# Performance work log

Hardware: AMD Instinct MI355X
Metric: run time of the kernel (lower is better)

Reference implementation:

```python
import jax, jax.numpy as jnp
import numpy as np

N = 10000        # num_nodes
E = 160000       # num_edges (before self loops)
D_IN = 256       # input_dim
H = 128          # hidden_dim (= per-head out_channels)
HEADS = 4
HD = HEADS * H   # 512
L = 16           # num_layers
OUT = 1024       # output_dim
G = 8            # num graphs in batch
EPS = 1e-5


def _layer_norm(x, w, b):
    m = jnp.mean(x, axis=-1, keepdims=True)
    v = jnp.mean(jnp.square(x - m), axis=-1, keepdims=True)
    return (x - m) / jnp.sqrt(v + EPS) * w + b


def setup_inputs() -> dict:
    key = jax.random.key(0)
    ks = jax.random.split(key, 20)
    s = 0.05
    x = jax.random.normal(ks[0], (N, D_IN), jnp.float32)
    edge_index = jax.random.randint(ks[1], (2, E), 0, N, dtype=jnp.int64)
    batch = jnp.sort(jax.random.randint(ks[2], (N,), 0, G, dtype=jnp.int64))
    return {
        "x": x,
        "edge_index": edge_index,
        "batch": batch,
        "W_in": jax.random.normal(ks[3], (D_IN, H), jnp.float32) * s,
        "b_in": jnp.zeros((H,), jnp.float32),
        "ln_in_w": jnp.ones((H,), jnp.float32),
        "ln_in_b": jnp.zeros((H,), jnp.float32),
        "Wsrc": jax.random.normal(ks[4], (L, H, HD), jnp.float32) * s,
        "Wdst": jax.random.normal(ks[5], (L, H, HD), jnp.float32) * s,
        "att_src": jax.random.normal(ks[6], (L, HEADS, H), jnp.float32) * s,
        "att_dst": jax.random.normal(ks[7], (L, HEADS, H), jnp.float32) * s,
        "Wout": jax.random.normal(ks[8], (L, HD, H), jnp.float32) * s,
        "bout": jnp.zeros((L, H), jnp.float32),
        "ln_w": jnp.ones((L, H), jnp.float32),
        "ln_b": jnp.zeros((L, H), jnp.float32),
        "Wp1": jax.random.normal(ks[9], (H, OUT), jnp.float32) * s,
        "bp1": jnp.zeros((OUT,), jnp.float32),
        "Wp2": jax.random.normal(ks[10], (OUT, OUT), jnp.float32) * s,
        "bp2": jnp.zeros((OUT,), jnp.float32),
    }


def reference(x, edge_index, batch, W_in, b_in, ln_in_w, ln_in_b,
              Wsrc, Wdst, att_src, att_dst, Wout, bout, ln_w, ln_b,
              Wp1, bp1, Wp2, bp2):
    # add self loops once (same edge set every layer)
    loop = jnp.arange(N, dtype=edge_index.dtype)
    e_src = jnp.concatenate([edge_index[0], loop])  # x_j (source)
    e_dst = jnp.concatenate([edge_index[1], loop])  # x_i (target / aggregate index)

    h = jax.nn.relu(_layer_norm(x @ W_in + b_in, ln_in_w, ln_in_b))  # [N, H]

    for l in range(L):
        hs = (h[e_src] @ Wsrc[l]).reshape(-1, HEADS, H)  # [E2, heads, H]
        hd = (h[e_dst] @ Wdst[l]).reshape(-1, HEADS, H)
        a = jnp.sum(hs * att_src[l], axis=-1) + jnp.sum(hd * att_dst[l], axis=-1)  # [E2, heads]
        a = jax.nn.leaky_relu(a, 0.2)
        # NOTE: faithful to source -- softmax over HEADS per edge, not over neighbors
        a = jax.nn.softmax(a, axis=-1)
        msg = (hs * a[..., None]).reshape(-1, HD)  # [E2, HD]
        agg = jax.ops.segment_sum(msg, e_dst, num_segments=N)  # [N, HD]
        out = agg @ Wout[l] + bout[l]
        h = jax.nn.relu(_layer_norm(out + h, ln_w[l], ln_b[l]))  # residual: H == H

    g = jax.ops.segment_max(h, batch, num_segments=G)  # global max pool [G, H]
    g = jax.nn.relu(g @ Wp1 + bp1)
    return g @ Wp2 + bp2  # [G, OUT]
```

## Files before the change

kernel.cpp:

```cpp
#include <hip/hip_runtime.h>
#include <hip/hip_bf16.h>

#define N_NODES 10000
#define E_EDGES 160000
#define E2 (E_EDGES + N_NODES)
#define D_IN 256
#define H 128
#define HEADS 4
#define HD 512
#define L_LAYERS 16
#define OUT_DIM 1024
#define G_GRAPHS 8
#define EPS 1e-5f
#define SPAD 10016

typedef unsigned short ushort_t;
typedef __attribute__((ext_vector_type(8))) short short8;
typedef __attribute__((ext_vector_type(4))) float f32x4;
typedef __attribute__((ext_vector_type(4))) unsigned u32x4;

__device__ __forceinline__ f32x4 mfma16(short8 a, short8 b, f32x4 c) {
    return __builtin_amdgcn_mfma_f32_16x16x32_bf16(a, b, c, 0, 0, 0);
}
__device__ __forceinline__ unsigned short f2b(float f) {
    unsigned u = __float_as_uint(f);
    u += 0x7fffu + ((u >> 16) & 1u);
    return (unsigned short)(u >> 16);
}
__device__ __forceinline__ float b2f(unsigned short b) {
    return __uint_as_float((unsigned)b << 16);
}
__device__ __forceinline__ unsigned pk2(float lo, float hi) {
    __hip_bfloat162 p = __float22bfloat162_rn(make_float2(lo, hi));
    return *(unsigned*)&p;
}

__global__ void k_zero(int* deg, int* cur, unsigned* g) {
    int i = blockIdx.x * blockDim.x + threadIdx.x;
    if (i < N_NODES) { deg[i] = 0; cur[i] = 0; }
    if (i < G_GRAPHS * H) g[i] = 0u;
}

__global__ void k_count(const int* ei, int* deg) {
    int e = blockIdx.x * blockDim.x + threadIdx.x;
    if (e >= E2) return;
    int d = (e < E_EDGES) ? ei[E_EDGES + e] : (e - E_EDGES);
    atomicAdd(&deg[d], 1);
}

__global__ void k_scan(const int* deg, int* rs) {
    __shared__ int s[1024];
    int t = threadIdx.x;
    int base = t * 10;
    int loc[10], run = 0;
    #pragma unroll
    for (int i = 0; i < 10; i++) {
        int idx = base + i;
        int v = (idx < N_NODES) ? deg[idx] : 0;
        loc[i] = run; run += v;
    }
    s[t] = run;
    __syncthreads();
    for (int off = 1; off < 1024; off <<= 1) {
        int xv = (t >= off) ? s[t - off] : 0;
        __syncthreads();
        s[t] += xv;
        __syncthreads();
    }
    int excl = s[t] - run;
    #pragma unroll
    for (int i = 0; i < 10; i++) {
        int idx = base + i;
        if (idx <= N_NODES) rs[idx] = excl + loc[i];
    }
}

__global__ void k_fill(const int* ei, const int* rs, int* cur, int* elist) {
    int e = blockIdx.x * blockDim.x + threadIdx.x;
    if (e >= E2) return;
    int s, d;
    if (e < E_EDGES) { s = ei[e]; d = ei[E_EDGES + e]; }
    else { s = d = e - E_EDGES; }
    int pos = atomicAdd(&cur[d], 1);
    elist[rs[d] + pos] = s;
}

__global__ void k_vw(const float* Wsrc, const float* Wdst,
                     const float* att_src, const float* att_dst,
                     float* vsrc, float* vdst) {
    int l = blockIdx.x;
    int t = threadIdx.x;
    int head = t >> 7, j = t & 127;
    const float* Ws = Wsrc + (size_t)l * H * HD;
    const float* Wd = Wdst + (size_t)l * H * HD;
    const float* As = att_src + (size_t)l * HEADS * H;
    const float* Ad = att_dst + (size_t)l * HEADS * H;
    float ss = 0.f, sd = 0.f;
    for (int k = 0; k < H; k++) {
        ss += Ws[(size_t)j * HD + head * H + k] * As[head * H + k];
        sd += Wd[(size_t)j * HD + head * H + k] * Ad[head * H + k];
    }
    vsrc[(size_t)l * HD + head * H + j] = ss;
    vdst[(size_t)l * HD + head * H + j] = sd;
}

__global__ __launch_bounds__(256) void k_mm(const float* __restrict__ Wsrc,
        const float* __restrict__ Wout, float* __restrict__ M) {
    __shared__ float As[32][33];
    __shared__ float Bs[32][128];
    int bid = blockIdx.x;
    int q = bid & 3, hh = (bid >> 2) & 3, l = bid >> 4;
    int t = threadIdx.x;
    int ty = t >> 4, tx = t & 15;
    const float* WsB = Wsrc + (size_t)l * H * HD + (size_t)hh * 128;
    const float* WoB = Wout + (size_t)l * HD * H + (size_t)hh * 128 * H;
    float acc[2][8];
    #pragma unroll
    for (int r = 0; r < 2; r++)
        #pragma unroll
        for (int c = 0; c < 8; c++) acc[r][c] = 0.f;
    for (int kt = 0; kt < 4; kt++) {
        #pragma unroll
        for (int i = 0; i < 4; i++) {
            int lin = i * 256 + t;
            int rr = lin >> 5, cc = lin & 31;
            As[rr][cc] = WsB[(size_t)(q * 32 + rr) * HD + kt * 32 + cc];
        }
        #pragma unroll
        for (int i = 0; i < 16; i++) {
            int lin = i * 256 + t;
            int rr = lin >> 7, cc = lin & 127;
            Bs[rr][cc] = WoB[(size_t)(kt * 32 + rr) * H + cc];
        }
        __syncthreads();
        #pragma unroll
        for (int kk = 0; kk < 32; kk++) {
            float a0 = As[ty * 2][kk], a1 = As[ty * 2 + 1][kk];
            float4 b0 = *(const float4*)&Bs[kk][tx * 8];
            float4 b1 = *(const float4*)&Bs[kk][tx * 8 + 4];
            acc[0][0] += a0 * b0.x; acc[0][1] += a0 * b0.y;
            acc[0][2] += a0 * b0.z; acc[0][3] += a0 * b0.w;
            acc[0][4] += a0 * b1.x; acc[0][5] += a0 * b1.y;
            acc[0][6] += a0 * b1.z; acc[0][7] += a0 * b1.w;
            acc[1][0] += a1 * b0.x; acc[1][1] += a1 * b0.y;
            acc[1][2] += a1 * b0.z; acc[1][3] += a1 * b0.w;
            acc[1][4] += a1 * b1.x; acc[1][5] += a1 * b1.y;
            acc[1][6] += a1 * b1.z; acc[1][7] += a1 * b1.w;
        }
        __syncthreads();
    }
    #pragma unroll
    for (int r = 0; r < 2; r++)
        #pragma unroll
        for (int c = 0; c < 8; c++)
            M[(size_t)l * HD * H + (size_t)(hh * 128 + q * 32 + ty * 2 + r) * H + tx * 8 + c]
                = acc[r][c];
}

__global__ void k_pack_out2(const float* M, ushort_t* Wh, ushort_t* Wl) {
    int idx = blockIdx.x * 256 + threadIdx.x;
    int l = idx >> 16, rem = idx & 65535;
    int k = rem >> 7, col = rem & 127;
    float v = M[(size_t)l * HD * H + (size_t)k * H + col];
    unsigned short hi = f2b(v);
    unsigned short lo = f2b(v - b2f(hi));
    int nt = col >> 4, ks = k >> 5, lhi = (k >> 3) & 3, llo = col & 15, j = k & 7;
    size_t addr = (size_t)l * 65536 + (((size_t)(nt * 16 + ks) * 64) + lhi * 16 + llo) * 8 + j;
    Wh[addr] = hi;
    Wl[addr] = lo;
}

__global__ void k_pack_win(const float* W, ushort_t* Wp) {
    int idx = blockIdx.x * 256 + threadIdx.x;
    int k = idx >> 7, col = idx & 127;
    float v = W[(size_t)k * H + col];
    int nt = col >> 4, ks = k >> 5, lhi = (k >> 3) & 3, llo = col & 15, j = k & 7;
    Wp[(((size_t)(nt * 8 + ks) * 64) + lhi * 16 + llo) * 8 + j] = f2b(v);
}

__global__ __launch_bounds__(256) void k_in_mfma(
        const float* __restrict__ x, const ushort_t* __restrict__ WpI,
        const float* __restrict__ b_in, const float* __restrict__ lnw,
        const float* __restrict__ lnb, const float* __restrict__ vs,
        const float* __restrict__ vd, float* __restrict__ as0, float* __restrict__ ad0,
        float* __restrict__ h, ushort_t* __restrict__ hb) {
    __shared__ float part1[4][16], part2[4][16];
    __shared__ float apart[4][8][16];
    int t = threadIdx.x, w = t >> 6, lane = t & 63;
    int row0 = blockIdx.x * 16;
    int ar = lane & 15, ac = (lane >> 4) * 8;
    short8 a[8];
    #pragma unroll
    for (int ks = 0; ks < 8; ks++) {
        const float* xp = x + (size_t)(row0 + ar) * D_IN + ks * 32 + ac;
        float4 xa = *(const float4*)xp;
        float4 xb = *(const float4*)(xp + 4);
        u32x4 u;
        u.x = pk2(xa.x, xa.y); u.y = pk2(xa.z, xa.w);
        u.z = pk2(xb.x, xb.y); u.w = pk2(xb.z, xb.w);
        a[ks] = *(short8*)&u;
    }
    const ushort_t* B0 = WpI + ((size_t)(w * 2 + 0) * 8) * 64 * 8;
    const ushort_t* B1 = WpI + ((size_t)(w * 2 + 1) * 8) * 64 * 8;
    f32x4 c0 = {0.f, 0.f, 0.f, 0.f}, c1 = {0.f, 0.f, 0.f, 0.f};
    #pragma unroll
    for (int ks = 0; ks < 8; ks++) {
        short8 b0 = *(const short8*)(B0 + ((size_t)ks * 64 + lane) * 8);
        short8 b1 = *(const short8*)(B1 + ((size_t)ks * 64 + lane) * 8);
        c0 = mfma16(a[ks], b0, c0);
        c1 = mfma16(a[ks], b1, c1);
    }
    int col0 = w * 32 + ar, col1 = w * 32 + 16 + ar;
    int rb = (lane >> 4) * 4;
    float v0[4], v1[4], y0[4], y1[4];
    #pragma unroll
    for (int r = 0; r < 4; r++) {
        v0[r] = c0[r] + b_in[col0];
        v1[r] = c1[r] + b_in[col1];
        float p1 = v0[r] + v1[r];
        float p2 = v0[r] * v0[r] + v1[r] * v1[r];
        #pragma unroll
        for (int off = 1; off < 16; off <<= 1) {
            p1 += __shfl_xor(p1, off);
            p2 += __shfl_xor(p2, off);
        }
        if (ar == 0) { part1[w][rb + r] = p1; part2[w][rb + r] = p2; }
    }
    __syncthreads();
    #pragma unroll
    for (int r = 0; r < 4; r++) {
        int lr = rb + r;
        int row = row0 + lr;
        float s1 = part1[0][lr] + part1[1][lr] + part1[2][lr] + part1[3][lr];
        float s2 = part2[0][lr] + part2[1][lr] + part2[2][lr] + part2[3][lr];
        float m = s1 * (1.f / 128.f);
        float var = s2 * (1.f / 128.f) - m * m;
        float is = rsqrtf(var + EPS);
        y0[r] = fmaxf((v0[r] - m) * is * lnw[col0] + lnb[col0], 0.f);
        y1[r] = fmaxf((v1[r] - m) * is * lnw[col1] + lnb[col1], 0.f);
        h[(size_t)row * H + col0] = y0[r];
        h[(size_t)row * H + col1] = y1[r];
        hb[(size_t)row * H + col0] = f2b(y0[r]);
        hb[(size_t)row * H + col1] = f2b(y1[r]);
    }
    #pragma unroll
    for (int comp = 0; comp < 8; comp++) {
        float vc0 = (comp < 4) ? vs[comp * H + col0] : vd[(comp - 4) * H + col0];
        float vc1 = (comp < 4) ? vs[comp * H + col1] : vd[(comp - 4) * H + col1];
        float p[4];
        #pragma unroll
        for (int r = 0; r < 4; r++) p[r] = y0[r] * vc0 + y1[r] * vc1;
        #pragma unroll
        for (int off = 1; off < 16; off <<= 1)
            #pragma unroll
            for (int r = 0; r < 4; r++) p[r] += __shfl_xor(p[r], off);
        if (ar == 0)
            #pragma unroll
            for (int r = 0; r < 4; r++) apart[w][comp][rb + r] = p[r];
    }
    __syncthreads();
    if (t < 128) {
        int lr = t >> 3, comp = t & 7;
        float s = apart[0][comp][lr] + apart[1][comp][lr]
                + apart[2][comp][lr] + apart[3][comp][lr];
        int node = row0 + lr;
        if (comp < 4) as0[node * 4 + comp] = s;
        else          ad0[node * 4 + comp - 4] = s;
    }
}

#define ACC1(uv, wt) do { \
    acc[0] += (wt) * __uint_as_float((uv).x << 16); \
    acc[1] += (wt) * __uint_as_float((uv).x & 0xffff0000u); \
    acc[2] += (wt) * __uint_as_float((uv).y << 16); \
    acc[3] += (wt) * __uint_as_float((uv).y & 0xffff0000u); \
    acc[4] += (wt) * __uint_as_float((uv).z << 16); \
    acc[5] += (wt) * __uint_as_float((uv).z & 0xffff0000u); \
    acc[6] += (wt) * __uint_as_float((uv).w << 16); \
    acc[7] += (wt) * __uint_as_float((uv).w & 0xffff0000u); \
} while (0)

__global__ __launch_bounds__(512) void k_aggout(
        const ushort_t* __restrict__ hb, const float4* __restrict__ as4,
        const float4* __restrict__ ad4, const int* __restrict__ rs,
        const int* __restrict__ elist, const ushort_t* __restrict__ Wh,
        const ushort_t* __restrict__ Wl, const float* __restrict__ bout,
        const float* __restrict__ lnw, const float* __restrict__ lnb,
        const float* __restrict__ vsn, const float* __restrict__ vdn,
        float* __restrict__ asn, float* __restrict__ adn, int doAlpha,
        float* __restrict__ h, ushort_t* __restrict__ hbo, int l) {
    __shared__ ushort_t frag[16 * 64 * 8];
    __shared__ int sl[8][64];
    __shared__ float wl[8][64][4];
    __shared__ float part1[8][16], part2[8][16];
    __shared__ float apart[8][8][16];
    int t = threadIdx.x, w = t >> 6, lane = t & 63;
    int base = blockIdx.x * 16;
    int head = lane >> 4;
    int j8 = (lane & 15) * 8;

    for (int q = 0; q < 2; q++) {
        int r = w * 2 + q;
        int node = base + r;
        int start = rs[node], end = rs[node + 1];
        float4 adv = ad4[node];
        float acc[8];
        #pragma unroll
        for (int i = 0; i < 8; i++) acc[i] = 0.f;
        for (int c0 = start; c0 < end; c0 += 64) {
            int cnt = min(64, end - c0);
            if (lane < cnt) {
                int s = elist[c0 + lane];
                sl[w][lane] = s;
                float4 av = as4[s];
                float l0 = av.x + adv.x, l1 = av.y + adv.y, l2 = av.z + adv.z, l3 = av.w + adv.w;
                l0 = (l0 > 0.f) ? l0 : 0.2f * l0;
                l1 = (l1 > 0.f) ? l1 : 0.2f * l1;
                l2 = (l2 > 0.f) ? l2 : 0.2f * l2;
                l3 = (l3 > 0.f) ? l3 : 0.2f * l3;
                float mx = fmaxf(fmaxf(l0, l1), fmaxf(l2, l3));
                float e0 = expf(l0 - mx), e1 = expf(l1 - mx), e2 = expf(l2 - mx), e3 = expf(l3 - mx);
                float inv = 1.f / (e0 + e1 + e2 + e3);
                wl[w][lane][0] = e0 * inv;
                wl[w][lane][1] = e1 * inv;
                wl[w][lane][2] = e2 * inv;
                wl[w][lane][3] = e3 * inv;
            }
            __asm__ volatile("s_waitcnt lgkmcnt(0)" ::: "memory");
            int j = 0;
            if (cnt >= 4) {
                u32x4 b0, b1, b2, b3;
                float q0, q1, q2, q3;
                {
                    int s0 = sl[w][0], s1 = sl[w][1], s2 = sl[w][2], s3 = sl[w][3];
                    q0 = wl[w][0][head]; q1 = wl[w][1][head];
                    q2 = wl[w][2][head]; q3 = wl[w][3][head];
                    b0 = *(const u32x4*)(hb + (size_t)s0 * H + j8);
                    b1 = *(const u32x4*)(hb + (size_t)s1 * H + j8);
                    b2 = *(const u32x4*)(hb + (size_t)s2 * H + j8);
                    b3 = *(const u32x4*)(hb + (size_t)s3 * H + j8);
                }
                for (j = 4; j + 3 < cnt; j += 4) {
                    int s0 = sl[w][j], s1 = sl[w][j + 1], s2 = sl[w][j + 2], s3 = sl[w][j + 3];
                    u32x4 n0 = *(const u32x4*)(hb + (size_t)s0 * H + j8);
                    u32x4 n1 = *(const u32x4*)(hb + (size_t)s1 * H + j8);
                    u32x4 n2 = *(const u32x4*)(hb + (size_t)s2 * H + j8);
                    u32x4 n3 = *(const u32x4*)(hb + (size_t)s3 * H + j8);
                    float r0 = wl[w][j][head], r1 = wl[w][j + 1][head];
                    float r2 = wl[w][j + 2][head], r3 = wl[w][j + 3][head];
                    ACC1(b0, q0); ACC1(b1, q1); ACC1(b2, q2); ACC1(b3, q3);
                    b0 = n0; q0 = r0; b1 = n1; q1 = r1;
                    b2 = n2; q2 = r2; b3 = n3; q3 = r3;
                }
                ACC1(b0, q0); ACC1(b1, q1); ACC1(b2, q2); ACC1(b3, q3);
            }
            for (; j < cnt; j++) {
                int s = sl[w][j];
                float wt = wl[w][j][head];
                u32x4 uv = *(const u32x4*)(hb + (size_t)s * H + j8);
                ACC1(uv, wt);
            }
        }
        u32x4 o;
        o.x = pk2(acc[0], acc[1]);
        o.y = pk2(acc[2], acc[3]);
        o.z = pk2(acc[4], acc[5]);
        o.w = pk2(acc[6], acc[7]);
        int ksn = head * 4 + ((lane >> 2) & 3);
        int gidx = ((lane & 3) * 16 + r) * 16 + (ksn ^ r);
        *(u32x4*)((char*)frag + gidx * 16) = o;
    }
    __syncthreads();

    const ushort_t* WLh = Wh + (size_t)l * 65536;
    const ushort_t* WLl = Wl + (size_t)l * 65536;
    short8 a[16];
    #pragma unroll
    for (int ks = 0; ks < 16; ks++) {
        int gidx = lane * 16 + (ks ^ (lane & 15));
        a[ks] = *(const short8*)((const char*)frag + gidx * 16);
    }
    int ar = lane & 15;
    f32x4 c = {0.f, 0.f, 0.f, 0.f};
    #pragma unroll
    for (int ks = 0; ks < 16; ks++) {
        short8 bh = *(const short8*)(WLh + ((size_t)(w * 16 + ks) * 64 + lane) * 8);
        c = mfma16(a[ks], bh, c);
    }
    #pragma unroll
    for (int ks = 0; ks < 16; ks++) {
        short8 bl = *(const short8*)(WLl + ((size_t)(w * 16 + ks) * 64 + lane) * 8);
        c = mfma16(a[ks], bl, c);
    }

    const float* bo = bout + (size_t)l * H;
    const float* gw = lnw + (size_t)l * H;
    const float* gb = lnb + (size_t)l * H;
    int col = w * 16 + ar;
    int rb = (lane >> 4) * 4;
    float v[4], y[4];
    #pragma unroll
    for (int r = 0; r < 4; r++) {
        int row = base + rb + r;
        v[r] = c[r] + bo[col] + h[(size_t)row * H + col];
        float p1 = v[r];
        float p2 = v[r] * v[r];
        #pragma unroll
        for (int off = 1; off < 16; off <<= 1) {
            p1 += __shfl_xor(p1, off);
            p2 += __shfl_xor(p2, off);
        }
        if (ar == 0) { part1[w][rb + r] = p1; part2[w][rb + r] = p2; }
    }
    __syncthreads();
    #pragma unroll
    for (int r = 0; r < 4; r++) {
        int lr = rb + r;
        int row = base + lr;
        float s1 = 0.f, s2 = 0.f;
        #pragma unroll
        for (int ww = 0; ww < 8; ww++) { s1 += part1[ww][lr]; s2 += part2[ww][lr]; }
        float m = s1 * (1.f / 128.f);
        float var = s2 * (1.f / 128.f) - m * m;
        float is = rsqrtf(var + EPS);
        y[r] = fmaxf((v[r] - m) * is * gw[col] + gb[col], 0.f);
        h[(size_t)row * H + col] = y[r];
        hbo[(size_t)row * H + col] = f2b(y[r]);
    }

    if (doAlpha) {
        #pragma unroll
        for (int comp = 0; comp < 8; comp++) {
            float vc = (comp < 4) ? vsn[comp * H + col] : vdn[(comp - 4) * H + col];
            float p[4];
            #pragma unroll
            for (int r = 0; r < 4; r++) p[r] = y[r] * vc;
            #pragma unroll
            for (int off = 1; off < 16; off <<= 1)
                #pragma unroll
                for (int r = 0; r < 4; r++) p[r] += __shfl_xor(p[r], off);
            if (ar == 0)
                #pragma unroll
                for (int r = 0; r < 4; r++) apart[w][comp][rb + r] = p[r];
        }
        __syncthreads();
        if (t < 128) {
            int lr = t >> 3, comp = t & 7;
            float s = 0.f;
            #pragma unroll
            for (int ww = 0; ww < 8; ww++) s += apart[ww][comp][lr];
            int node = base + lr;
            if (comp < 4) asn[node * 4 + comp] = s;
            else          adn[node * 4 + comp - 4] = s;
        }
    }
}

__global__ void k_pool(const float* __restrict__ h, const int* __restrict__ batch,
                       unsigned* __restrict__ g) {
    __shared__ float lm[G_GRAPHS][H];
    int t = threadIdx.x;
    #pragma unroll
    for (int i = 0; i < G_GRAPHS; i++) lm[i][t] = 0.f;
    int n0 = blockIdx.x * 100, n1 = n0 + 100;
    for (int n = n0; n < n1; n++) {
        int b = batch[n];
        lm[b][t] = fmaxf(lm[b][t], h[(size_t)n * H + t]);
    }
    #pragma unroll
    for (int i = 0; i < G_GRAPHS; i++)
        atomicMax(&g[i * H + t], __float_as_uint(lm[i][t]));
}

__global__ void k_mlp1(const unsigned* __restrict__ g, const float* __restrict__ Wp1,
                       const float* __restrict__ bp1, float* __restrict__ g1) {
    __shared__ float gs[H];
    int gr = blockIdx.x >> 2, ch = blockIdx.x & 3;
    int t = threadIdx.x;
    if (t < H) gs[t] = __uint_as_float(g[gr * H + t]);
    __syncthreads();
    int col = ch * 256 + t;
    float acc = 0.f;
    for (int k = 0; k < H; k++) acc += gs[k] * Wp1[(size_t)k * OUT_DIM + col];
    acc += bp1[col];
    g1[(size_t)gr * OUT_DIM + col] = fmaxf(acc, 0.f);
}

__global__ void k_mlp2(const float* __restrict__ g1, const float* __restrict__ Wp2,
                       const float* __restrict__ bp2, float* __restrict__ out) {
    __shared__ float gs[OUT_DIM];
    __shared__ float part[4][64];
    int gr = blockIdx.x >> 4, ch = blockIdx.x & 15;
    int t = threadIdx.x;
    int ci = t & 63, si = t >> 6;
    for (int i = t; i < OUT_DIM; i += 256) gs[i] = g1[(size_t)gr * OUT_DIM + i];
    __syncthreads();
    int col = ch * 64 + ci;
    float acc = 0.f;
    for (int k = si * 256; k < si * 256 + 256; k++)
        acc += gs[k] * Wp2[(size_t)k * OUT_DIM + col];
    part[si][ci] = acc;
    __syncthreads();
    if (si == 0) {
        float r = part[0][ci] + part[1][ci] + part[2][ci] + part[3][ci] + bp2[col];
        out[(size_t)gr * OUT_DIM + col] = r;
    }
}

extern "C" void kernel_launch(void* const* d_in, const int* in_sizes, int n_in,
                              void* d_out, int out_size, void* d_ws, size_t ws_size,
                              hipStream_t stream) {
    const float* x       = (const float*)d_in[0];
    const int*   ei      = (const int*)d_in[1];
    const int*   batch   = (const int*)d_in[2];
    const float* W_in    = (const float*)d_in[3];
    const float* b_in    = (const float*)d_in[4];
    const float* ln_in_w = (const float*)d_in[5];
    const float* ln_in_b = (const float*)d_in[6];
    const float* Wsrc    = (const float*)d_in[7];
    const float* Wdst    = (const float*)d_in[8];
    const float* att_src = (const float*)d_in[9];
    const float* att_dst = (const float*)d_in[10];
    const float* Wout    = (const float*)d_in[11];
    const float* bout    = (const float*)d_in[12];
    const float* ln_w    = (const float*)d_in[13];
    const float* ln_b    = (const float*)d_in[14];
    const float* Wp1     = (const float*)d_in[15];
    const float* bp1     = (const float*)d_in[16];
    const float* Wp2     = (const float*)d_in[17];
    const float* bp2     = (const float*)d_in[18];

    char* w = (char*)d_ws;
    auto alloc = [&](size_t bytes) { void* p = w; w += (bytes + 255) & ~(size_t)255; return p; };
    float*     h     = (float*)alloc((size_t)N_NODES * H * 4);
    ushort_t*  hb0   = (ushort_t*)alloc((size_t)SPAD * H * 2);
    ushort_t*  hb1   = (ushort_t*)alloc((size_t)SPAD * H * 2);
    float*     as0   = (float*)alloc((size_t)SPAD * HEADS * 4);
    float*     ad0   = (float*)alloc((size_t)SPAD * HEADS * 4);
    float*     as1   = (float*)alloc((size_t)SPAD * HEADS * 4);
    float*     ad1   = (float*)alloc((size_t)SPAD * HEADS * 4);
    float*     vsrc  = (float*)alloc((size_t)L_LAYERS * HD * 4);
    float*     vdst  = (float*)alloc((size_t)L_LAYERS * HD * 4);
    float*     M     = (float*)alloc((size_t)L_LAYERS * HD * H * 4);
    ushort_t*  WpH   = (ushort_t*)alloc((size_t)L_LAYERS * 65536 * 2);
    ushort_t*  WpL   = (ushort_t*)alloc((size_t)L_LAYERS * 65536 * 2);
    ushort_t*  WpI   = (ushort_t*)alloc((size_t)D_IN * H * 2);
    int*       deg   = (int*)alloc((size_t)N_NODES * 4);
    int*       rs    = (int*)alloc((size_t)(N_NODES + 1) * 4);
    int*       cur   = (int*)alloc((size_t)N_NODES * 4);
    int*       elist = (int*)alloc((size_t)E2 * 4);
    unsigned*  g     = (unsigned*)alloc((size_t)G_GRAPHS * H * 4);
    float*     g1    = (float*)alloc((size_t)G_GRAPHS * OUT_DIM * 4);

    k_zero<<<40, 256, 0, stream>>>(deg, cur, g);
    k_count<<<(E2 + 255) / 256, 256, 0, stream>>>(ei, deg);
    k_scan<<<1, 1024, 0, stream>>>(deg, rs);
    k_fill<<<(E2 + 255) / 256, 256, 0, stream>>>(ei, rs, cur, elist);
    k_vw<<<L_LAYERS, 512, 0, stream>>>(Wsrc, Wdst, att_src, att_dst, vsrc, vdst);
    k_mm<<<256, 256, 0, stream>>>(Wsrc, Wout, M);
    k_pack_out2<<<4096, 256, 0, stream>>>(M, WpH, WpL);
    k_pack_win<<<128, 256, 0, stream>>>(W_in, WpI);
    k_in_mfma<<<N_NODES / 16, 256, 0, stream>>>(x, WpI, b_in, ln_in_w, ln_in_b,
                                                vsrc, vdst, as0, ad0, h, hb0);

    for (int l = 0; l < L_LAYERS; l++) {
        const ushort_t* hbi = (l & 1) ? hb1 : hb0;
        ushort_t*       hbo = (l & 1) ? hb0 : hb1;
        const float* aA = (l & 1) ? as1 : as0;
        const float* dA = (l & 1) ? ad1 : ad0;
        float* aB = (l & 1) ? as0 : as1;
        float* dB = (l & 1) ? ad0 : ad1;
        int ln = (l + 1 < L_LAYERS) ? (l + 1) : (L_LAYERS - 1);
        k_aggout<<<N_NODES / 16, 512, 0, stream>>>(
            hbi, (const float4*)aA, (const float4*)dA, rs, elist, WpH, WpL,
            bout, ln_w, ln_b, vsrc + (size_t)ln * HD, vdst + (size_t)ln * HD,
            aB, dB, (l + 1 < L_LAYERS) ? 1 : 0, h, hbo, l);
    }

    k_pool<<<100, 128, 0, stream>>>(h, batch, g);
    k_mlp1<<<G_GRAPHS * 4, 256, 0, stream>>>(g, Wp1, bp1, g1);
    k_mlp2<<<G_GRAPHS * 16, 256, 0, stream>>>(g1, Wp2, bp2, (float*)d_out);
}
```

Measured before the change: 708.0 us.

## Split fused aggregate+projection kernel into separate gather and MFMA post kernels

Replaces the fused per-layer k_aggout kernel with two kernels. k_gather runs one wavefront per node, has each lane load a source row once and accumulate it into all four heads. It writes the aggregated [N,512] bf16 tensor to a global buffer T. k_post then reads T and runs the MFMA projection, layer norm and next-layer alpha computation, with each wave producing 32 columns. The intent is to cut redundant per-head gathers of neighbour rows and decouple gather occupancy from the MFMA stage, at the cost of an extra global round-trip of T and a second launch per layer.

New measurement: 723.7 us. 2.2% more time.

```diff
diff --git a/kernel.cpp b/kernel.cpp
--- a/kernel.cpp
+++ b/kernel.cpp
@@ -269,142 +269,132 @@
     }
 }
 
-#define ACC1(uv, wt) do { \
-    acc[0] += (wt) * __uint_as_float((uv).x << 16); \
-    acc[1] += (wt) * __uint_as_float((uv).x & 0xffff0000u); \
-    acc[2] += (wt) * __uint_as_float((uv).y << 16); \
-    acc[3] += (wt) * __uint_as_float((uv).y & 0xffff0000u); \
-    acc[4] += (wt) * __uint_as_float((uv).z << 16); \
-    acc[5] += (wt) * __uint_as_float((uv).z & 0xffff0000u); \
-    acc[6] += (wt) * __uint_as_float((uv).w << 16); \
-    acc[7] += (wt) * __uint_as_float((uv).w & 0xffff0000u); \
-} while (0)
-
-__global__ __launch_bounds__(512) void k_aggout(
+__global__ __launch_bounds__(256) void k_gather(
         const ushort_t* __restrict__ hb, const float4* __restrict__ as4,
         const float4* __restrict__ ad4, const int* __restrict__ rs,
-        const int* __restrict__ elist, const ushort_t* __restrict__ Wh,
+        const int* __restrict__ elist, ushort_t* __restrict__ T) {
+    __shared__ int sl[4][64];
+    __shared__ float wl[4][64][4];
+    int t = threadIdx.x, w = t >> 6, lane = t & 63;
+    int node = blockIdx.x * 4 + w;
+    int start = rs[node], end = rs[node + 1];
+    float4 adv = ad4[node];
+    int g = lane >> 4, i = lane & 15;
+    float acc0[8], acc1[8], acc2[8], acc3[8];
+    #pragma unroll
+    for (int c = 0; c < 8; c++) { acc0[c] = 0.f; acc1[c] = 0.f; acc2[c] = 0.f; acc3[c] = 0.f; }
+    for (int c0 = start; c0 < end; c0 += 64) {
+        int cnt = min(64, end - c0);
+        if (lane < cnt) {
+            int s = elist[c0 + lane];
+            sl[w][lane] = s;
+            float4 av = as4[s];
+            float l0 = av.x + adv.x, l1 = av.y + adv.y, l2 = av.z + adv.z, l3 = av.w + adv.w;
+            l0 = (l0 > 0.f) ? l0 : 0.2f * l0;
+            l1 = (l1 > 0.f) ? l1 : 0.2f * l1;
+            l2 = (l2 > 0.f) ? l2 : 0.2f * l2;
+            l3 = (l3 > 0.f) ? l3 : 0.2f * l3;
+            float mx = fmaxf(fmaxf(l0, l1), fmaxf(l2, l3));
+            float e0 = expf(l0 - mx), e1 = expf(l1 - mx), e2 = expf(l2 - mx), e3 = expf(l3 - mx);
+            float inv = 1.f / (e0 + e1 + e2 + e3);
+            wl[w][lane][0] = e0 * inv;
+            wl[w][lane][1] = e1 * inv;
+            wl[w][lane][2] = e2 * inv;
+            wl[w][lane][3] = e3 * inv;
+        } else {
+            sl[w][lane] = 0;
+            wl[w][lane][0] = 0.f; wl[w][lane][1] = 0.f;
+            wl[w][lane][2] = 0.f; wl[w][lane][3] = 0.f;
+        }
+        __asm__ volatile("s_waitcnt lgkmcnt(0)" ::: "memory");
+        int rounds = (cnt + 3) >> 2;
+        for (int jj = 0; jj < rounds; jj++) {
+            int j = jj * 4 + g;
+            int s = sl[w][j];
+            float4 wt = *(const float4*)wl[w][j];
+            u32x4 uv = *(const u32x4*)(hb + (size_t)s * H + i * 8);
+            float f0 = __uint_as_float(uv.x << 16);
+            float f1 = __uint_as_float(uv.x & 0xffff0000u);
+            float f2 = __uint_as_float(uv.y << 16);
+            float f3 = __uint_as_float(uv.y & 0xffff0000u);
+            float f4 = __uint_as_float(uv.z << 16);
+            float f5 = __uint_as_float(uv.z & 0xffff0000u);
+            float f6 = __uint_as_float(uv.w << 16);
+            float f7 = __uint_as_float(uv.w & 0xffff0000u);
+            acc0[0] += wt.x * f0; acc0[1] += wt.x * f1; acc0[2] += wt.x * f2; acc0[3] += wt.x * f3;
+            acc0[4] += wt.x * f4; acc0[5] += wt.x * f5; acc0[6] += wt.x * f6; acc0[7] += wt.x * f7;
+            acc1[0] += wt.y * f0; acc1[1] += wt.y * f1; acc1[2] += wt.y * f2; acc1[3] += wt.y * f3;
+            acc1[4] += wt.y * f4; acc1[5] += wt.y * f5; acc1[6] += wt.y * f6; acc1[7] += wt.y * f7;
+            acc2[0] += wt.z * f0; acc2[1] += wt.z * f1; acc2[2] += wt.z * f2; acc2[3] += wt.z * f3;
+            acc2[4] += wt.z * f4; acc2[5] += wt.z * f5; acc2[6] += wt.z * f6; acc2[7] += wt.z * f7;
+            acc3[0] += wt.w * f0; acc3[1] += wt.w * f1; acc3[2] += wt.w * f2; acc3[3] += wt.w * f3;
+            acc3[4] += wt.w * f4; acc3[5] += wt.w * f5; acc3[6] += wt.w * f6; acc3[7] += wt.w * f7;
+        }
+    }
+    float out[8];
+    #pragma unroll
+    for (int c = 0; c < 8; c++) {
+        float v0 = acc0[c], v1 = acc1[c], v2 = acc2[c], v3 = acc3[c];
+        v0 += __shfl_xor(v0, 16); v0 += __shfl_xor(v0, 32);
+        v1 += __shfl_xor(v1, 16); v1 += __shfl_xor(v1, 32);
+        v2 += __shfl_xor(v2, 16); v2 += __shfl_xor(v2, 32);
+        v3 += __shfl_xor(v3, 16); v3 += __shfl_xor(v3, 32);
+        out[c] = (g == 0) ? v0 : ((g == 1) ? v1 : ((g == 2) ? v2 : v3));
+    }
+    u32x4 o;
+    o.x = pk2(out[0], out[1]);
+    o.y = pk2(out[2], out[3]);
+    o.z = pk2(out[4], out[5]);
+    o.w = pk2(out[6], out[7]);
+    *(u32x4*)(T + (size_t)node * HD + g * 128 + i * 8) = o;
+}
+
+__global__ __launch_bounds__(256) void k_post(
+        const ushort_t* __restrict__ T, const ushort_t* __restrict__ Wh,
         const ushort_t* __restrict__ Wl, const float* __restrict__ bout,
         const float* __restrict__ lnw, const float* __restrict__ lnb,
         const float* __restrict__ vsn, const float* __restrict__ vdn,
         float* __restrict__ asn, float* __restrict__ adn, int doAlpha,
         float* __restrict__ h, ushort_t* __restrict__ hbo, int l) {
-    __shared__ ushort_t frag[16 * 64 * 8];
-    __shared__ int sl[8][64];
-    __shared__ float wl[8][64][4];
-    __shared__ float part1[8][16], part2[8][16];
-    __shared__ float apart[8][8][16];
+    __shared__ float part1[4][16], part2[4][16];
+    __shared__ float apart[4][8][16];
     int t = threadIdx.x, w = t >> 6, lane = t & 63;
-    int base = blockIdx.x * 16;
-    int head = lane >> 4;
-    int j8 = (lane & 15) * 8;
-
-    for (int q = 0; q < 2; q++) {
-        int r = w * 2 + q;
-        int node = base + r;
-        int start = rs[node], end = rs[node + 1];
-        float4 adv = ad4[node];
-        float acc[8];
-        #pragma unroll
-        for (int i = 0; i < 8; i++) acc[i] = 0.f;
-        for (int c0 = start; c0 < end; c0 += 64) {
-            int cnt = min(64, end - c0);
-            if (lane < cnt) {
-                int s = elist[c0 + lane];
-                sl[w][lane] = s;
-                float4 av = as4[s];
-                float l0 = av.x + adv.x, l1 = av.y + adv.y, l2 = av.z + adv.z, l3 = av.w + adv.w;
-                l0 = (l0 > 0.f) ? l0 : 0.2f * l0;
-                l1 = (l1 > 0.f) ? l1 : 0.2f * l1;
-                l2 = (l2 > 0.f) ? l2 : 0.2f * l2;
-                l3 = (l3 > 0.f) ? l3 : 0.2f * l3;
-                float mx = fmaxf(fmaxf(l0, l1), fmaxf(l2, l3));
-                float e0 = expf(l0 - mx), e1 = expf(l1 - mx), e2 = expf(l2 - mx), e3 = expf(l3 - mx);
-                float inv = 1.f / (e0 + e1 + e2 + e3);
-                wl[w][lane][0] = e0 * inv;
-                wl[w][lane][1] = e1 * inv;
-                wl[w][lane][2] = e2 * inv;
-                wl[w][lane][3] = e3 * inv;
-            }
-            __asm__ volatile("s_waitcnt lgkmcnt(0)" ::: "memory");
-            int j = 0;
-            if (cnt >= 4) {
-                u32x4 b0, b1, b2, b3;
-                float q0, q1, q2, q3;
-                {
-                    int s0 = sl[w][0], s1 = sl[w][1], s2 = sl[w][2], s3 = sl[w][3];
-                    q0 = wl[w][0][head]; q1 = wl[w][1][head];
-                    q2 = wl[w][2][head]; q3 = wl[w][3][head];
-                    b0 = *(const u32x4*)(hb + (size_t)s0 * H + j8);
-                    b1 = *(const u32x4*)(hb + (size_t)s1 * H + j8);
-                    b2 = *(const u32x4*)(hb + (size_t)s2 * H + j8);
-                    b3 = *(const u32x4*)(hb + (size_t)s3 * H + j8);
-                }
-                for (j = 4; j + 3 < cnt; j += 4) {
-                    int s0 = sl[w][j], s1 = sl[w][j + 1], s2 = sl[w][j + 2], s3 = sl[w][j + 3];
-                    u32x4 n0 = *(const u32x4*)(hb + (size_t)s0 * H + j8);
-                    u32x4 n1 = *(const u32x4*)(hb + (size_t)s1 * H + j8);
-                    u32x4 n2 = *(const u32x4*)(hb + (size_t)s2 * H + j8);
-                    u32x4 n3 = *(const u32x4*)(hb + (size_t)s3 * H + j8);
-                    float r0 = wl[w][j][head], r1 = wl[w][j + 1][head];
-                    float r2 = wl[w][j + 2][head], r3 = wl[w][j + 3][head];
-                    ACC1(b0, q0); ACC1(b1, q1); ACC1(b2, q2); ACC1(b3, q3);
-                    b0 = n0; q0 = r0; b1 = n1; q1 = r1;
-                    b2 = n2; q2 = r2; b3 = n3; q3 = r3;
-                }
-                ACC1(b0, q0); ACC1(b1, q1); ACC1(b2, q2); ACC1(b3, q3);
-            }
-            for (; j < cnt; j++) {
-                int s = sl[w][j];
-                float wt = wl[w][j][head];
-                u32x4 uv = *(const u32x4*)(hb + (size_t)s * H + j8);
-                ACC1(uv, wt);
-            }
-        }
-        u32x4 o;
-        o.x = pk2(acc[0], acc[1]);
-        o.y = pk2(acc[2], acc[3]);
-        o.z = pk2(acc[4], acc[5]);
-        o.w = pk2(acc[6], acc[7]);
-        int ksn = head * 4 + ((lane >> 2) & 3);
-        int gidx = ((lane & 3) * 16 + r) * 16 + (ksn ^ r);
-        *(u32x4*)((char*)frag + gidx * 16) = o;
-    }
-    __syncthreads();
-
+    int row0 = blockIdx.x * 16;
+    int ar = lane & 15, ac = (lane >> 4) * 8;
+    short8 a[16];
+    #pragma unroll
+    for (int ks = 0; ks < 16; ks++)
+        a[ks] = *(const short8*)(T + (size_t)(row0 + ar) * HD + ks * 32 + ac);
     const ushort_t* WLh = Wh + (size_t)l * 65536;
     const ushort_t* WLl = Wl + (size_t)l * 65536;
-    short8 a[16];
+    f32x4 c0 = {0.f, 0.f, 0.f, 0.f}, c1 = {0.f, 0.f, 0.f, 0.f};
     #pragma unroll
     for (int ks = 0; ks < 16; ks++) {
-        int gidx = lane * 16 + (ks ^ (lane & 15));
-        a[ks] = *(const short8*)((const char*)frag + gidx * 16);
-    }
-    int ar = lane & 15;
-    f32x4 c = {0.f, 0.f, 0.f, 0.f};
+        short8 b0 = *(const short8*)(WLh + ((size_t)((w * 2 + 0) * 16 + ks) * 64 + lane) * 8);
+        short8 b1 = *(const short8*)(WLh + ((size_t)((w * 2 + 1) * 16 + ks) * 64 + lane) * 8);
+        c0 = mfma16(a[ks], b0, c0);
+        c1 = mfma16(a[ks], b1, c1);
+    }
     #pragma unroll
     for (int ks = 0; ks < 16; ks++) {
-        short8 bh = *(const short8*)(WLh + ((size_t)(w * 16 + ks) * 64 + lane) * 8);
-        c = mfma16(a[ks], bh, c);
-    }
-    #pragma unroll
-    for (int ks = 0; ks < 16; ks++) {
-        short8 bl = *(const short8*)(WLl + ((size_t)(w * 16 + ks) * 64 + lane) * 8);
-        c = mfma16(a[ks], bl, c);
-    }
-
+        short8 b0 = *(const short8*)(WLl + ((size_t)((w * 2 + 0) * 16 + ks) * 64 + lane) * 8);
+        short8 b1 = *(const short8*)(WLl + ((size_t)((w * 2 + 1) * 16 + ks) * 64 + lane) * 8);
+        c0 = mfma16(a[ks], b0, c0);
+        c1 = mfma16(a[ks], b1, c1);
+    }
     const float* bo = bout + (size_t)l * H;
     const float* gw = lnw + (size_t)l * H;
     const float* gb = lnb + (size_t)l * H;
-    int col = w * 16 + ar;
+    int col0 = w * 32 + ar, col1 = w * 32 + 16 + ar;
     int rb = (lane >> 4) * 4;
-    float v[4], y[4];
+    float v0[4], v1[4], y0[4], y1[4];
     #pragma unroll
     for (int r = 0; r < 4; r++) {
-        int row = base + rb + r;
-        v[r] = c[r] + bo[col] + h[(size_t)row * H + col];
-        float p1 = v[r];
-        float p2 = v[r] * v[r];
+        int row = row0 + rb + r;
+        v0[r] = c0[r] + bo[col0] + h[(size_t)row * H + col0];
+        v1[r] = c1[r] + bo[col1] + h[(size_t)row * H + col1];
+        float p1 = v0[r] + v1[r];
+        float p2 = v0[r] * v0[r] + v1[r] * v1[r];
         #pragma unroll
         for (int off = 1; off < 16; off <<= 1) {
             p1 += __shfl_xor(p1, off);
@@ -416,25 +406,27 @@
     #pragma unroll
     for (int r = 0; r < 4; r++) {
         int lr = rb + r;
-        int row = base + lr;
-        float s1 = 0.f, s2 = 0.f;
-        #pragma unroll
-        for (int ww = 0; ww < 8; ww++) { s1 += part1[ww][lr]; s2 += part2[ww][lr]; }
+        int row = row0 + lr;
+        float s1 = part1[0][lr] + part1[1][lr] + part1[2][lr] + part1[3][lr];
+        float s2 = part2[0][lr] + part2[1][lr] + part2[2][lr] + part2[3][lr];
         float m = s1 * (1.f / 128.f);
         float var = s2 * (1.f / 128.f) - m * m;
         float is = rsqrtf(var + EPS);
-        y[r] = fmaxf((v[r] - m) * is * gw[col] + gb[col], 0.f);
-        h[(size_t)row * H + col] = y[r];
-        hbo[(size_t)row * H + col] = f2b(y[r]);
-    }
-
+        y0[r] = fmaxf((v0[r] - m) * is * gw[col0] + gb[col0], 0.f);
+        y1[r] = fmaxf((v1[r] - m) * is * gw[col1] + gb[col1], 0.f);
+        h[(size_t)row * H + col0] = y0[r];
+        h[(size_t)row * H + col1] = y1[r];
+        hbo[(size_t)row * H + col0] = f2b(y0[r]);
+        hbo[(size_t)row * H + col1] = f2b(y1[r]);
+    }
     if (doAlpha) {
         #pragma unroll
         for (int comp = 0; comp < 8; comp++) {
-            float vc = (comp < 4) ? vsn[comp * H + col] : vdn[(comp - 4) * H + col];
+            float vc0 = (comp < 4) ? vsn[comp * H + col0] : vdn[(comp - 4) * H + col0];
+            float vc1 = (comp < 4) ? vsn[comp * H + col1] : vdn[(comp - 4) * H + col1];
             float p[4];
             #pragma unroll
-            for (int r = 0; r < 4; r++) p[r] = y[r] * vc;
+            for (int r = 0; r < 4; r++) p[r] = y0[r] * vc0 + y1[r] * vc1;
             #pragma unroll
             for (int off = 1; off < 16; off <<= 1)
                 #pragma unroll
@@ -446,10 +438,9 @@
         __syncthreads();
         if (t < 128) {
             int lr = t >> 3, comp = t & 7;
-            float s = 0.f;
-            #pragma unroll
-            for (int ww = 0; ww < 8; ww++) s += apart[ww][comp][lr];
-            int node = base + lr;
+            float s = apart[0][comp][lr] + apart[1][comp][lr]
+                    + apart[2][comp][lr] + apart[3][comp][lr];
+            int node = row0 + lr;
             if (comp < 4) asn[node * 4 + comp] = s;
             else          adn[node * 4 + comp - 4] = s;
         }
@@ -535,6 +526,7 @@
     float*     h     = (float*)alloc((size_t)N_NODES * H * 4);
     ushort_t*  hb0   = (ushort_t*)alloc((size_t)SPAD * H * 2);
     ushort_t*  hb1   = (ushort_t*)alloc((size_t)SPAD * H * 2);
+    ushort_t*  T     = (ushort_t*)alloc((size_t)SPAD * HD * 2);
     float*     as0   = (float*)alloc((size_t)SPAD * HEADS * 4);
     float*     ad0   = (float*)alloc((size_t)SPAD * HEADS * 4);
     float*     as1   = (float*)alloc((size_t)SPAD * HEADS * 4);
@@ -571,9 +563,11 @@
         float* aB = (l & 1) ? as0 : as1;
         float* dB = (l & 1) ? ad0 : ad1;
         int ln = (l + 1 < L_LAYERS) ? (l + 1) : (L_LAYERS - 1);
-        k_aggout<<<N_NODES / 16, 512, 0, stream>>>(
-            hbi, (const float4*)aA, (const float4*)dA, rs, elist, WpH, WpL,
-            bout, ln_w, ln_b, vsrc + (size_t)ln * HD, vdst + (size_t)ln * HD,
+        k_gather<<<N_NODES / 4, 256, 0, stream>>>(hbi, (const float4*)aA, (const float4*)dA,
+                                                  rs, elist, T);
+        k_post<<<N_NODES / 16, 256, 0, stream>>>(
+            T, WpH, WpL, bout, ln_w, ln_b,
+            vsrc + (size_t)ln * HD, vdst + (size_t)ln * HD,
             aB, dB, (l + 1 < L_LAYERS) ? 1 : 0, h, hbo, l);
     }
 
```
